# Kernel tuning notes

Measured on AMD Instinct MI355X. Metric: run time of the kernel, lower is better.

The kernel has to match this reference:

```python
import jax, jax.numpy as jnp
import numpy as np

N, E, D, H, G, C = 50000, 800000, 128, 128, 256, 10
BN_EPS = 1e-5

def _lin_init(key, fan_in, fan_out):
    k1, k2 = jax.random.split(key)
    bound = 1.0 / np.sqrt(fan_in)
    w = jax.random.uniform(k1, (fan_in, fan_out), jnp.float32, -bound, bound)
    b = jax.random.uniform(k2, (fan_out,), jnp.float32, -bound, bound)
    return w, b

def setup_inputs() -> dict:
    key = jax.random.key(0)
    ks = jax.random.split(key, 16)
    x = jax.random.normal(ks[0], (N, D), jnp.float32)
    edge_index = jax.random.randint(ks[1], (2, E), 0, N, jnp.int64)
    batch = jnp.sort(jax.random.randint(ks[2], (N,), 0, G, jnp.int64))
    inp = {"x": x, "edge_index": edge_index, "batch": batch}
    # per-layer GIN MLP params: Linear-ReLU-Linear-ReLU-BN
    dims = [(D, H), (H, H), (H, H)]
    for i, (din, dh) in enumerate(dims, start=1):
        wa, ba = _lin_init(ks[2 + 2 * i], din, dh)
        wb, bb = _lin_init(ks[3 + 2 * i], dh, dh)
        inp[f"w{i}a"], inp[f"b{i}a"] = wa, ba
        inp[f"w{i}b"], inp[f"b{i}b"] = wb, bb
        inp[f"g{i}"] = jnp.ones((dh,), jnp.float32)
        inp[f"bt{i}"] = jnp.zeros((dh,), jnp.float32)
    inp["eps"] = jnp.zeros((3,), jnp.float32)  # train_eps=True, init 0
    inp["lw1"], inp["lb1"] = _lin_init(ks[10], H, H)
    inp["lw2"], inp["lb2"] = _lin_init(ks[11], H, C)
    return inp

def _gin_layer(x, src, dst, eps_i, wa, ba, wb, bb, g, bt):
    # scatter-add neighbor aggregation: out[i] = sum_{j->i} x[j]
    agg = jax.ops.segment_sum(x[src], dst, num_segments=N)
    h = (1.0 + eps_i) * x + agg
    h = jax.nn.relu(h @ wa + ba)
    h = jax.nn.relu(h @ wb + bb)
    mu = h.mean(axis=0)
    var = ((h - mu) ** 2).mean(axis=0)  # biased var (torch BN normalization)
    return g * (h - mu) * jax.lax.rsqrt(var + BN_EPS) + bt

def reference(x, edge_index, batch, w1a, b1a, w1b, b1b, g1, bt1,
              w2a, b2a, w2b, b2b, g2, bt2, w3a, b3a, w3b, b3b, g3, bt3,
              eps, lw1, lb1, lw2, lb2):
    src, dst = edge_index[0], edge_index[1]
    h = _gin_layer(x, src, dst, eps[0], w1a, b1a, w1b, b1b, g1, bt1)
    h = _gin_layer(h, src, dst, eps[1], w2a, b2a, w2b, b2b, g2, bt2)
    h = _gin_layer(h, src, dst, eps[2], w3a, b3a, w3b, b3b, g3, bt3)
    # global mean pool over batch ids
    sums = jax.ops.segment_sum(h, batch, num_segments=G)
    cnt = jax.ops.segment_sum(jnp.ones((N,), h.dtype), batch, num_segments=G)
    pooled = sums / jnp.maximum(cnt, 1.0)[:, None]
    z = jax.nn.relu(pooled @ lw1 + lb1)
    # dropout omitted (eval / deterministic reference)
    z = z @ lw2 + lb2
    return jax.nn.log_softmax(z, axis=-1)
```

## Files before the change

### kernel.cpp

```cpp
#include <hip/hip_runtime.h>

#define N_NODES 50000
#define N_EDGES 800000
#define DIM 128
#define N_GRAPHS 256
#define N_CLS 10
#define BN_EPSV 1e-5f
#define CAP 64
#define RSIZE 6250
#define NBLK ((N_NODES + 63) / 64)
#define ZROW N_NODES

typedef __attribute__((ext_vector_type(8))) short short8;
typedef __attribute__((ext_vector_type(4))) float f32x4;

__device__ __forceinline__ float bf2f(short u) {
  return __uint_as_float(((unsigned)(unsigned short)u) << 16);
}
__device__ __forceinline__ unsigned short f2bf(float f) {
  unsigned u = __float_as_uint(f);
  unsigned r = (u + 0x7FFFu + ((u >> 16) & 1u)) >> 16;
  return (unsigned short)r;
}
__device__ __forceinline__ int swz(int row, int bytecol) {
  return row * 256 + (bytecol ^ ((row & 7) << 4));
}


__global__ __launch_bounds__(256) void prep_kernel(
    const float* __restrict__ x, ushort* __restrict__ xb,
    const float* __restrict__ w0, const float* __restrict__ w1,
    const float* __restrict__ w2, const float* __restrict__ w3,
    const float* __restrict__ w4, const float* __restrict__ w5,
    ushort* __restrict__ wt, const int* __restrict__ batch,
    int* __restrict__ gstart, int* __restrict__ cnt,
    ushort* __restrict__ z0, ushort* __restrict__ z1) {
  int bid = blockIdx.x, tid = threadIdx.x;
  if (bid < 384) {
    int m = bid >> 6;
    const float* w = m == 0 ? w0 : m == 1 ? w1 : m == 2 ? w2 : m == 3 ? w3
                                                         : m == 4 ? w4 : w5;
    int idx = (bid & 63) * 256 + tid;
    int k = idx >> 7, n = idx & 127;
    wt[m * 16384 + n * 128 + k] = f2bf(w[idx]);
  } else if (bid < 384 + 2048) {
    const int tot = N_NODES * DIM / 4;
    int i = (bid - 384) * 256 + tid;
    for (; i < tot; i += 2048 * 256) {
      float4 v = ((const float4*)x)[i];
      ushort4 o;
      o.x = f2bf(v.x); o.y = f2bf(v.y); o.z = f2bf(v.z); o.w = f2bf(v.w);
      ((ushort4*)xb)[i] = o;
    }
  } else if (bid < 384 + 2048 + 196) {
    int i = (bid - (384 + 2048)) * 256 + tid;
    if (i < N_NODES) {
      cnt[i] = 0;
      int b = batch[i];
      int prev = (i == 0) ? -1 : batch[i - 1];
      for (int g = prev + 1; g <= b; g++) gstart[g] = i;
      if (i == N_NODES - 1)
        for (int g = b + 1; g <= N_GRAPHS; g++) gstart[g] = N_NODES;
    }
  } else {
    if (tid < DIM) {
      z0[(size_t)ZROW * DIM + tid] = 0;
      z1[(size_t)ZROW * DIM + tid] = 0;
    }
  }
}


__global__ __launch_bounds__(256) void fill_kernel(
    const int* __restrict__ src, const int* __restrict__ dst,
    int* __restrict__ cnt, ushort* __restrict__ csr) {
  int cls = blockIdx.x & 7;
  int lo = cls * RSIZE;
  int hi = lo + RSIZE;
  int i = (blockIdx.x >> 3) * blockDim.x + threadIdx.x;
  int stride = (gridDim.x >> 3) * blockDim.x;
  for (; i < N_EDGES; i += stride) {
    int d = dst[i];
    if (d >= lo && d < hi) {
      int p = atomicAdd(&cnt[d], 1);
      if (p < CAP) csr[(size_t)d * CAP + p] = (ushort)src[i];
    }
  }
}


template <bool FIRST>
__global__ __launch_bounds__(512, 8) void layer_kernel(
    const ushort* __restrict__ xin, const int* __restrict__ cnt,
    const ushort* __restrict__ csr, const float* __restrict__ pstats,
    const float* __restrict__ pgamma, const float* __restrict__ pbeta,
    const float* __restrict__ epsp, int layer,
    const ushort* __restrict__ W1T, const float* __restrict__ b1,
    const ushort* __restrict__ W2T, const float* __restrict__ b2,
    ushort* __restrict__ out, float* __restrict__ bstat) {
  __shared__ __align__(16) ushort As[64 * DIM];
  __shared__ __align__(16) ushort H1[64 * DIM];
  __shared__ float sums[8 * DIM];
  __shared__ float sqs[8 * DIM];
  int tid = threadIdx.x;
  int w8 = tid >> 6;
  int l = tid & 63, li = l & 15, lg = l >> 4;
  int row0 = blockIdx.x * 64;
  float epv = 1.0f + epsp[layer];
  if (!FIRST) {
    if (tid < DIM) {
      const float invN = 1.0f / N_NODES;
      float mu = pstats[tid] * invN;
      float var = fmaxf(pstats[DIM + tid] * invN - mu * mu, 0.f);
      float sc = pgamma[tid] * rsqrtf(var + BN_EPSV);
      sums[tid] = sc;
      sqs[tid] = pbeta[tid] - mu * sc;
    }
    __syncthreads();
  }
  for (int n = 0; n < 8; n++) {
    int nl = w8 * 8 + n;
    int node = row0 + nl;
    float av[8];
#pragma unroll
    for (int j = 0; j < 8; j++) av[j] = 0.f;
    if (node < N_NODES) {
      int deg = cnt[node];
      deg = deg < CAP ? deg : CAP;
      const ushort* nb = csr + (size_t)node * CAP;
      if (lg == 0) {
        short8 sv = *(const short8*)(xin + (size_t)node * DIM + li * 8);
#pragma unroll
        for (int j = 0; j < 8; j++) av[j] = epv * bf2f(sv[j]);
      }
      int nbat = (deg + 15) >> 4;
      for (int b = 0; b < nbat; b++) {
        int i0 = b * 16 + lg, i1 = i0 + 4, i2 = i0 + 8, i3 = i0 + 12;
        int r0 = nb[i0 < deg ? i0 : 0];
        int r1 = nb[i1 < deg ? i1 : 0];
        int r2 = nb[i2 < deg ? i2 : 0];
        int r3 = nb[i3 < deg ? i3 : 0];
        int j0 = i0 < deg ? r0 : ZROW;
        int j1 = i1 < deg ? r1 : ZROW;
        int j2 = i2 < deg ? r2 : ZROW;
        int j3 = i3 < deg ? r3 : ZROW;
        short8 v0 = *(const short8*)(xin + (size_t)j0 * DIM + li * 8);
        short8 v1 = *(const short8*)(xin + (size_t)j1 * DIM + li * 8);
        short8 v2 = *(const short8*)(xin + (size_t)j2 * DIM + li * 8);
        short8 v3 = *(const short8*)(xin + (size_t)j3 * DIM + li * 8);
#pragma unroll
        for (int j = 0; j < 8; j++)
          av[j] += (bf2f(v0[j]) + bf2f(v1[j])) + (bf2f(v2[j]) + bf2f(v3[j]));
      }
#pragma unroll
      for (int j = 0; j < 8; j++) {
        av[j] += __shfl_xor(av[j], 16, 64);
        av[j] += __shfl_xor(av[j], 32, 64);
      }
      if (!FIRST && lg == 0) {
        float co = epv + (float)deg;
#pragma unroll
        for (int j = 0; j < 8; j++)
          av[j] = sums[li * 8 + j] * av[j] + co * sqs[li * 8 + j];
      }
    }
    if (lg == 0) {
      short8 uv;
#pragma unroll
      for (int j = 0; j < 8; j++) uv[j] = (short)f2bf(av[j]);
      *(short8*)((char*)As + swz(nl, li * 16)) = uv;
    }
  }
  __syncthreads();
  int wg = w8 >> 1;
  int ch = w8 & 1;
  {
    f32x4 acc[4] = {};
    short8 af[4];
#pragma unroll
    for (int ks = 0; ks < 4; ks++)
      af[ks] = *(const short8*)((char*)As + swz(16 * wg + li, ks * 64 + lg * 16));
#pragma unroll
    for (int ct4 = 0; ct4 < 4; ct4++) {
      int ct = ch * 4 + ct4;
      const char* wp = (const char*)W1T + (ct * 16 + li) * 256 + lg * 16;
#pragma unroll
      for (int ks = 0; ks < 4; ks++) {
        short8 bf = *(const short8*)(wp + ks * 64);
        acc[ct4] = __builtin_amdgcn_mfma_f32_16x16x32_bf16(af[ks], bf, acc[ct4], 0, 0, 0);
      }
    }
#pragma unroll
    for (int ct4 = 0; ct4 < 4; ct4++) {
      int ct = ch * 4 + ct4;
      float bv = b1[ct * 16 + li];
#pragma unroll
      for (int r = 0; r < 4; r++) {
        int row = 16 * wg + lg * 4 + r;
        *(ushort*)((char*)H1 + swz(row, (ct * 16 + li) * 2)) =
            f2bf(fmaxf(acc[ct4][r] + bv, 0.f));
      }
    }
  }
  __syncthreads();
  float ss[4] = {0, 0, 0, 0}, sq[4] = {0, 0, 0, 0};
  {
    f32x4 acc[4] = {};
    short8 af[4];
#pragma unroll
    for (int ks = 0; ks < 4; ks++)
      af[ks] = *(const short8*)((char*)H1 + swz(16 * wg + li, ks * 64 + lg * 16));
#pragma unroll
    for (int ct4 = 0; ct4 < 4; ct4++) {
      int ct = ch * 4 + ct4;
      const char* wp = (const char*)W2T + (ct * 16 + li) * 256 + lg * 16;
#pragma unroll
      for (int ks = 0; ks < 4; ks++) {
        short8 bf = *(const short8*)(wp + ks * 64);
        acc[ct4] = __builtin_amdgcn_mfma_f32_16x16x32_bf16(af[ks], bf, acc[ct4], 0, 0, 0);
      }
    }
#pragma unroll
    for (int ct4 = 0; ct4 < 4; ct4++) {
      int ct = ch * 4 + ct4;
      float bv = b2[ct * 16 + li];
#pragma unroll
      for (int r = 0; r < 4; r++) {
        int row = 16 * wg + lg * 4 + r;
        float v = fmaxf(acc[ct4][r] + bv, 0.f);
        *(ushort*)((char*)As + swz(row, (ct * 16 + li) * 2)) = f2bf(v);
        float vm = (row0 + row < N_NODES) ? v : 0.f;
        ss[ct4] += vm;
        sq[ct4] += vm * vm;
      }
    }
  }
#pragma unroll
  for (int ct4 = 0; ct4 < 4; ct4++) {
    ss[ct4] += __shfl_xor(ss[ct4], 16, 64);
    ss[ct4] += __shfl_xor(ss[ct4], 32, 64);
    sq[ct4] += __shfl_xor(sq[ct4], 16, 64);
    sq[ct4] += __shfl_xor(sq[ct4], 32, 64);
  }
  if (l < 16) {
#pragma unroll
    for (int ct4 = 0; ct4 < 4; ct4++) {
      sums[w8 * DIM + (ch * 4 + ct4) * 16 + l] = ss[ct4];
      sqs[w8 * DIM + (ch * 4 + ct4) * 16 + l] = sq[ct4];
      sums[w8 * DIM + ((1 - ch) * 4 + ct4) * 16 + l] = 0.f;
      sqs[w8 * DIM + ((1 - ch) * 4 + ct4) * 16 + l] = 0.f;
    }
  }
  __syncthreads();
  for (int t = tid; t < 1024; t += 512) {
    int row = t >> 4, chunk = t & 15;
    int grow = row0 + row;
    if (grow < N_NODES) {
      short8 v = *(const short8*)((char*)As + swz(row, chunk * 16));
      *(short8*)(out + (size_t)grow * DIM + chunk * 8) = v;
    }
  }
  if (tid < DIM) {
    float t1 = 0.f, t2 = 0.f;
#pragma unroll
    for (int g = 0; g < 8; g++) {
      t1 += sums[g * DIM + tid];
      t2 += sqs[g * DIM + tid];
    }
    bstat[(size_t)blockIdx.x * DIM + tid] = t1;
    bstat[((size_t)NBLK + blockIdx.x) * DIM + tid] = t2;
  }
}


__global__ __launch_bounds__(64) void stats_reduce_kernel(
    const float* __restrict__ bstat, float* __restrict__ stats) {
  int c = blockIdx.x;
  int t = threadIdx.x;
  const float* src = bstat + (c < DIM ? 0 : (size_t)NBLK * DIM) + (c & (DIM - 1));
  float a = 0.f;
  for (int b = t; b < NBLK; b += 64) a += src[(size_t)b * DIM];
#pragma unroll
  for (int m = 32; m >= 1; m >>= 1) a += __shfl_xor(a, m, 64);
  if (t == 0) stats[c] = a;
}


__global__ __launch_bounds__(128) void pool2_kernel(const ushort* __restrict__ h,
    const int* __restrict__ gstart, float* __restrict__ pool) {
  int g = blockIdx.x, t = threadIdx.x;
  int s = gstart[g], e = gstart[g + 1];
  float a0 = 0.f, a1 = 0.f, a2 = 0.f, a3 = 0.f;
  int i = s;
  for (; i + 3 < e; i += 4) {
    a0 += bf2f((short)h[(size_t)(i + 0) * DIM + t]);
    a1 += bf2f((short)h[(size_t)(i + 1) * DIM + t]);
    a2 += bf2f((short)h[(size_t)(i + 2) * DIM + t]);
    a3 += bf2f((short)h[(size_t)(i + 3) * DIM + t]);
  }
  for (; i < e; i++) a0 += bf2f((short)h[(size_t)i * DIM + t]);
  float cn = (float)(e - s);
  if (cn < 1.f) cn = 1.f;
  pool[g * DIM + t] = ((a0 + a1) + (a2 + a3)) / cn;
}


__global__ __launch_bounds__(128) void final_kernel(const float* __restrict__ pool,
    const float* __restrict__ stats3,
    const float* __restrict__ gamma3, const float* __restrict__ beta3,
    const float* __restrict__ lw1, const float* __restrict__ lb1,
    const float* __restrict__ lw2, const float* __restrict__ lb2,
    float* __restrict__ out) {
  int g = blockIdx.x, t = threadIdx.x;
  __shared__ float p[DIM];
  __shared__ float part[2];
  __shared__ float z2[N_CLS];
  const float invN = 1.0f / N_NODES;
  float mu = stats3[t] * invN;
  float var = fmaxf(stats3[DIM + t] * invN - mu * mu, 0.f);
  float sc = gamma3[t] * rsqrtf(var + BN_EPSV);
  float sh = beta3[t] - mu * sc;
  p[t] = sc * pool[g * DIM + t] + sh;
  __syncthreads();
  float acc = lb1[t];
  for (int k = 0; k < DIM; k++) acc += p[k] * lw1[k * DIM + t];
  acc = fmaxf(acc, 0.f);
  for (int c = 0; c < N_CLS; c++) {
    float v = acc * lw2[t * N_CLS + c];
#pragma unroll
    for (int m = 32; m >= 1; m >>= 1) v += __shfl_xor(v, m, 64);
    if ((t & 63) == 0) part[t >> 6] = v;
    __syncthreads();
    if (t == 0) z2[c] = part[0] + part[1] + lb2[c];
    __syncthreads();
  }
  if (t == 0) {
    float mx = -1e30f;
    for (int c = 0; c < N_CLS; c++) mx = fmaxf(mx, z2[c]);
    float sum = 0.f;
    for (int c = 0; c < N_CLS; c++) sum += expf(z2[c] - mx);
    float lse = mx + logf(sum);
    for (int c = 0; c < N_CLS; c++) out[g * N_CLS + c] = z2[c] - lse;
  }
}


extern "C" void kernel_launch(void* const* d_in, const int* in_sizes, int n_in,
                              void* d_out, int out_size, void* d_ws, size_t ws_size,
                              hipStream_t stream) {
  const float* x = (const float*)d_in[0];
  const int* edge = (const int*)d_in[1];
  const int* batch = (const int*)d_in[2];
  const float *w[3][2], *bv[3][2], *gam[3], *bet[3];
  int idx = 3;
  for (int l = 0; l < 3; l++) {
    w[l][0] = (const float*)d_in[idx++]; bv[l][0] = (const float*)d_in[idx++];
    w[l][1] = (const float*)d_in[idx++]; bv[l][1] = (const float*)d_in[idx++];
    gam[l] = (const float*)d_in[idx++];  bet[l] = (const float*)d_in[idx++];
  }
  const float* eps = (const float*)d_in[idx++];
  const float* lw1 = (const float*)d_in[idx++];
  const float* lb1 = (const float*)d_in[idx++];
  const float* lw2 = (const float*)d_in[idx++];
  const float* lb2 = (const float*)d_in[idx++];

  char* ws = (char*)d_ws;
  size_t off_b = 0;
  auto alloc = [&](size_t b) -> char* {
    char* p = ws + off_b;
    off_b += (b + 255) & ~(size_t)255;
    return p;
  };
  int* cnt = (int*)alloc((size_t)N_NODES * 4);
  ushort* csr = (ushort*)alloc((size_t)N_NODES * CAP * 2);
  ushort* P0 = (ushort*)alloc((size_t)(N_NODES + 1) * DIM * 2);
  ushort* P1 = (ushort*)alloc((size_t)(N_NODES + 1) * DIM * 2);
  ushort* wt = (ushort*)alloc((size_t)6 * 16384 * 2);
  float* stats = (float*)alloc(3 * 2 * DIM * 4);
  float* pool = (float*)alloc((size_t)N_GRAPHS * DIM * 4);
  int* gstart = (int*)alloc((size_t)(N_GRAPHS + 1) * 4);
  float* bstat = (float*)alloc((size_t)2 * NBLK * DIM * 4);

  const int* srcp = edge;
  const int* dstp = edge + N_EDGES;
  prep_kernel<<<384 + 2048 + 196 + 1, 256, 0, stream>>>(
      x, P0, w[0][0], w[0][1], w[1][0], w[1][1], w[2][0], w[2][1], wt,
      batch, gstart, cnt, P0, P1);
  fill_kernel<<<2048, 256, 0, stream>>>(srcp, dstp, cnt, csr);

  layer_kernel<true><<<NBLK, 512, 0, stream>>>(
      P0, cnt, csr, nullptr, nullptr, nullptr, eps, 0,
      wt + 0 * 16384, bv[0][0], wt + 1 * 16384, bv[0][1], P1, bstat);
  stats_reduce_kernel<<<256, 64, 0, stream>>>(bstat, stats);
  layer_kernel<false><<<NBLK, 512, 0, stream>>>(
      P1, cnt, csr, stats, gam[0], bet[0], eps, 1,
      wt + 2 * 16384, bv[1][0], wt + 3 * 16384, bv[1][1], P0, bstat);
  stats_reduce_kernel<<<256, 64, 0, stream>>>(bstat, stats + 2 * DIM);
  layer_kernel<false><<<NBLK, 512, 0, stream>>>(
      P0, cnt, csr, stats + 2 * DIM, gam[1], bet[1], eps, 2,
      wt + 4 * 16384, bv[2][0], wt + 5 * 16384, bv[2][1], P1, bstat);
  stats_reduce_kernel<<<256, 64, 0, stream>>>(bstat, stats + 4 * DIM);

  pool2_kernel<<<N_GRAPHS, 128, 0, stream>>>(P1, gstart, pool);
  final_kernel<<<N_GRAPHS, 128, 0, stream>>>(pool, stats + 4 * DIM,
                                             gam[2], bet[2], lw1, lb1, lw2, lb2,
                                             (float*)d_out);
}
```

Measured before the change: 278.0 us.

## Split aggregation from MLP and store features in column-sliced layout

Node features are stored as eight 16-column slices (32 bytes per node per slice), and the fused layer kernel is split into a separate aggregation kernel and an MFMA MLP kernel. Each aggregation block works on one slice, chosen by blockIdx & 7, so each slice's working set is small enough to stay cache-resident during the random neighbor gathers. The cost is an extra round trip of the aggregated features through global memory, one more launch per layer, and smaller 8-byte gathers per lane.

```diff
diff --git a/kernel.cpp b/kernel.cpp
--- a/kernel.cpp
+++ b/kernel.cpp
@@ -10,6 +10,8 @@
 #define RSIZE 6250
 #define NBLK ((N_NODES + 63) / 64)
 #define ZROW N_NODES
+#define SLICE ((N_NODES + 1) * 16)
+#define AGG_WPC 768
 
 typedef __attribute__((ext_vector_type(8))) short short8;
 typedef __attribute__((ext_vector_type(4))) float f32x4;
@@ -43,17 +45,24 @@
     int idx = (bid & 63) * 256 + tid;
     int k = idx >> 7, n = idx & 127;
     wt[m * 16384 + n * 128 + k] = f2bf(w[idx]);
-  } else if (bid < 384 + 2048) {
-    const int tot = N_NODES * DIM / 4;
-    int i = (bid - 384) * 256 + tid;
-    for (; i < tot; i += 2048 * 256) {
-      float4 v = ((const float4*)x)[i];
-      ushort4 o;
-      o.x = f2bf(v.x); o.y = f2bf(v.y); o.z = f2bf(v.z); o.w = f2bf(v.w);
-      ((ushort4*)xb)[i] = o;
-    }
-  } else if (bid < 384 + 2048 + 196) {
-    int i = (bid - (384 + 2048)) * 256 + tid;
+  } else if (bid < 384 + 3125) {
+    int id = (bid - 384) * 256 + tid;
+    if (id < 8 * N_NODES * 2) {
+      int s = id / (N_NODES * 2);
+      int r = id - s * (N_NODES * 2);
+      int node = r >> 1, h = r & 1;
+      const float* src = x + (size_t)node * DIM + s * 16 + h * 8;
+      float4 a = *(const float4*)src;
+      float4 b = *(const float4*)(src + 4);
+      short8 o;
+      o[0] = (short)f2bf(a.x); o[1] = (short)f2bf(a.y);
+      o[2] = (short)f2bf(a.z); o[3] = (short)f2bf(a.w);
+      o[4] = (short)f2bf(b.x); o[5] = (short)f2bf(b.y);
+      o[6] = (short)f2bf(b.z); o[7] = (short)f2bf(b.w);
+      *(short8*)(xb + (size_t)s * SLICE + node * 16 + h * 8) = o;
+    }
+  } else if (bid < 384 + 3125 + 196) {
+    int i = (bid - (384 + 3125)) * 256 + tid;
     if (i < N_NODES) {
       cnt[i] = 0;
       int b = batch[i];
@@ -63,9 +72,10 @@
         for (int g = b + 1; g <= N_GRAPHS; g++) gstart[g] = N_NODES;
     }
   } else {
-    if (tid < DIM) {
-      z0[(size_t)ZROW * DIM + tid] = 0;
-      z1[(size_t)ZROW * DIM + tid] = 0;
+    if (tid < 128) {
+      int s = tid >> 4, cc = tid & 15;
+      z0[(size_t)s * SLICE + (size_t)ZROW * 16 + cc] = 0;
+      z1[(size_t)s * SLICE + (size_t)ZROW * 16 + cc] = 0;
     }
   }
 }
@@ -90,14 +100,102 @@
 
 
 template <bool FIRST>
-__global__ __launch_bounds__(512, 8) void layer_kernel(
+__global__ __launch_bounds__(256, 6) void agg_kernel(
     const ushort* __restrict__ xin, const int* __restrict__ cnt,
     const ushort* __restrict__ csr, const float* __restrict__ pstats,
     const float* __restrict__ pgamma, const float* __restrict__ pbeta,
-    const float* __restrict__ epsp, int layer,
-    const ushort* __restrict__ W1T, const float* __restrict__ b1,
-    const ushort* __restrict__ W2T, const float* __restrict__ b2,
-    ushort* __restrict__ out, float* __restrict__ bstat) {
+    const float* __restrict__ epsp, int layer, ushort* __restrict__ agg) {
+  int c = blockIdx.x & 7;
+  int wv = (blockIdx.x >> 3) * 4 + (threadIdx.x >> 6);
+  int l = threadIdx.x & 63;
+  int slot = l >> 2, colq = l & 3;
+  const ushort* F = xin + (size_t)c * SLICE;
+  ushort* A = agg + (size_t)c * SLICE;
+  float epv = 1.0f + epsp[layer];
+  float sc4[4], sh4[4];
+  if (!FIRST) {
+    const float invN = 1.0f / N_NODES;
+#pragma unroll
+    for (int j = 0; j < 4; j++) {
+      int col = c * 16 + colq * 4 + j;
+      float mu = pstats[col] * invN;
+      float var = fmaxf(pstats[DIM + col] * invN - mu * mu, 0.f);
+      float s = pgamma[col] * rsqrtf(var + BN_EPSV);
+      sc4[j] = s;
+      sh4[j] = pbeta[col] - mu * s;
+    }
+  }
+  for (int nb0 = wv; nb0 < N_NODES; nb0 += AGG_WPC * 4) {
+    int n_[4], d_[4];
+#pragma unroll
+    for (int q = 0; q < 4; q++) {
+      n_[q] = nb0 + AGG_WPC * q;
+      int valid = n_[q] < N_NODES;
+      int ndc = valid ? n_[q] : 0;
+      int dd = cnt[ndc];
+      dd = dd < CAP ? dd : CAP;
+      d_[q] = valid ? dd : 0;
+    }
+    int dmax = max(max(d_[0], d_[1]), max(d_[2], d_[3]));
+    int nbat = (dmax + 15) >> 4;
+    float av[4][4];
+#pragma unroll
+    for (int q = 0; q < 4; q++)
+#pragma unroll
+      for (int j = 0; j < 4; j++) av[q][j] = 0.f;
+    for (int b = 0; b < nbat; b++) {
+      int si = b * 16 + slot;
+#pragma unroll
+      for (int q = 0; q < 4; q++) {
+        int ndc = n_[q] < N_NODES ? n_[q] : 0;
+        int e = csr[(size_t)ndc * CAP + (si < d_[q] ? si : 0)];
+        int j = si < d_[q] ? e : ZROW;
+        ushort4 p = *(const ushort4*)(F + j * 16 + colq * 4);
+        av[q][0] += bf2f((short)p.x);
+        av[q][1] += bf2f((short)p.y);
+        av[q][2] += bf2f((short)p.z);
+        av[q][3] += bf2f((short)p.w);
+      }
+    }
+#pragma unroll
+    for (int q = 0; q < 4; q++)
+#pragma unroll
+      for (int j = 0; j < 4; j++) {
+        av[q][j] += __shfl_xor(av[q][j], 4, 64);
+        av[q][j] += __shfl_xor(av[q][j], 8, 64);
+        av[q][j] += __shfl_xor(av[q][j], 16, 64);
+        av[q][j] += __shfl_xor(av[q][j], 32, 64);
+      }
+    if (slot == 0) {
+#pragma unroll
+      for (int q = 0; q < 4; q++) {
+        if (n_[q] >= N_NODES) continue;
+        ushort4 sv = *(const ushort4*)(F + n_[q] * 16 + colq * 4);
+        float o0 = epv * bf2f((short)sv.x) + av[q][0];
+        float o1 = epv * bf2f((short)sv.y) + av[q][1];
+        float o2 = epv * bf2f((short)sv.z) + av[q][2];
+        float o3 = epv * bf2f((short)sv.w) + av[q][3];
+        if (!FIRST) {
+          float co = epv + (float)d_[q];
+          o0 = sc4[0] * o0 + co * sh4[0];
+          o1 = sc4[1] * o1 + co * sh4[1];
+          o2 = sc4[2] * o2 + co * sh4[2];
+          o3 = sc4[3] * o3 + co * sh4[3];
+        }
+        ushort4 ov;
+        ov.x = f2bf(o0); ov.y = f2bf(o1); ov.z = f2bf(o2); ov.w = f2bf(o3);
+        *(ushort4*)(A + n_[q] * 16 + colq * 4) = ov;
+      }
+    }
+  }
+}
+
+
+__global__ __launch_bounds__(512, 8) void mlp_kernel(
+    const ushort* __restrict__ agg, const ushort* __restrict__ W1T,
+    const float* __restrict__ b1, const ushort* __restrict__ W2T,
+    const float* __restrict__ b2, ushort* __restrict__ out,
+    float* __restrict__ bstat) {
   __shared__ __align__(16) ushort As[64 * DIM];
   __shared__ __align__(16) ushort H1[64 * DIM];
   __shared__ float sums[8 * DIM];
@@ -106,70 +204,14 @@
   int w8 = tid >> 6;
   int l = tid & 63, li = l & 15, lg = l >> 4;
   int row0 = blockIdx.x * 64;
-  float epv = 1.0f + epsp[layer];
-  if (!FIRST) {
-    if (tid < DIM) {
-      const float invN = 1.0f / N_NODES;
-      float mu = pstats[tid] * invN;
-      float var = fmaxf(pstats[DIM + tid] * invN - mu * mu, 0.f);
-      float sc = pgamma[tid] * rsqrtf(var + BN_EPSV);
-      sums[tid] = sc;
-      sqs[tid] = pbeta[tid] - mu * sc;
-    }
-    __syncthreads();
-  }
-  for (int n = 0; n < 8; n++) {
-    int nl = w8 * 8 + n;
-    int node = row0 + nl;
-    float av[8];
-#pragma unroll
-    for (int j = 0; j < 8; j++) av[j] = 0.f;
-    if (node < N_NODES) {
-      int deg = cnt[node];
-      deg = deg < CAP ? deg : CAP;
-      const ushort* nb = csr + (size_t)node * CAP;
-      if (lg == 0) {
-        short8 sv = *(const short8*)(xin + (size_t)node * DIM + li * 8);
-#pragma unroll
-        for (int j = 0; j < 8; j++) av[j] = epv * bf2f(sv[j]);
-      }
-      int nbat = (deg + 15) >> 4;
-      for (int b = 0; b < nbat; b++) {
-        int i0 = b * 16 + lg, i1 = i0 + 4, i2 = i0 + 8, i3 = i0 + 12;
-        int r0 = nb[i0 < deg ? i0 : 0];
-        int r1 = nb[i1 < deg ? i1 : 0];
-        int r2 = nb[i2 < deg ? i2 : 0];
-        int r3 = nb[i3 < deg ? i3 : 0];
-        int j0 = i0 < deg ? r0 : ZROW;
-        int j1 = i1 < deg ? r1 : ZROW;
-        int j2 = i2 < deg ? r2 : ZROW;
-        int j3 = i3 < deg ? r3 : ZROW;
-        short8 v0 = *(const short8*)(xin + (size_t)j0 * DIM + li * 8);
-        short8 v1 = *(const short8*)(xin + (size_t)j1 * DIM + li * 8);
-        short8 v2 = *(const short8*)(xin + (size_t)j2 * DIM + li * 8);
-        short8 v3 = *(const short8*)(xin + (size_t)j3 * DIM + li * 8);
-#pragma unroll
-        for (int j = 0; j < 8; j++)
-          av[j] += (bf2f(v0[j]) + bf2f(v1[j])) + (bf2f(v2[j]) + bf2f(v3[j]));
-      }
-#pragma unroll
-      for (int j = 0; j < 8; j++) {
-        av[j] += __shfl_xor(av[j], 16, 64);
-        av[j] += __shfl_xor(av[j], 32, 64);
-      }
-      if (!FIRST && lg == 0) {
-        float co = epv + (float)deg;
-#pragma unroll
-        for (int j = 0; j < 8; j++)
-          av[j] = sums[li * 8 + j] * av[j] + co * sqs[li * 8 + j];
-      }
-    }
-    if (lg == 0) {
-      short8 uv;
-#pragma unroll
-      for (int j = 0; j < 8; j++) uv[j] = (short)f2bf(av[j]);
-      *(short8*)((char*)As + swz(nl, li * 16)) = uv;
-    }
+  for (int t = tid; t < 1024; t += 512) {
+    int s = t >> 7, idx = t & 127;
+    int nl = idx >> 1, h = idx & 1;
+    int grow = row0 + nl;
+    short8 v = {};
+    if (grow < N_NODES)
+      v = *(const short8*)(agg + (size_t)s * SLICE + grow * 16 + h * 8);
+    *(short8*)((char*)As + swz(nl, s * 32 + h * 16)) = v;
   }
   __syncthreads();
   int wg = w8 >> 1;
@@ -253,11 +295,12 @@
   }
   __syncthreads();
   for (int t = tid; t < 1024; t += 512) {
-    int row = t >> 4, chunk = t & 15;
-    int grow = row0 + row;
+    int s = t >> 7, idx = t & 127;
+    int nl = idx >> 1, h = idx & 1;
+    int grow = row0 + nl;
     if (grow < N_NODES) {
-      short8 v = *(const short8*)((char*)As + swz(row, chunk * 16));
-      *(short8*)(out + (size_t)grow * DIM + chunk * 8) = v;
+      short8 v = *(const short8*)((char*)As + swz(nl, s * 32 + h * 16));
+      *(short8*)(out + (size_t)s * SLICE + grow * 16 + h * 8) = v;
     }
   }
   if (tid < DIM) {
@@ -289,17 +332,19 @@
 __global__ __launch_bounds__(128) void pool2_kernel(const ushort* __restrict__ h,
     const int* __restrict__ gstart, float* __restrict__ pool) {
   int g = blockIdx.x, t = threadIdx.x;
-  int s = gstart[g], e = gstart[g + 1];
+  int s = t >> 4, cc = t & 15;
+  const ushort* H = h + (size_t)s * SLICE + cc;
+  int st = gstart[g], e = gstart[g + 1];
   float a0 = 0.f, a1 = 0.f, a2 = 0.f, a3 = 0.f;
-  int i = s;
+  int i = st;
   for (; i + 3 < e; i += 4) {
-    a0 += bf2f((short)h[(size_t)(i + 0) * DIM + t]);
-    a1 += bf2f((short)h[(size_t)(i + 1) * DIM + t]);
-    a2 += bf2f((short)h[(size_t)(i + 2) * DIM + t]);
-    a3 += bf2f((short)h[(size_t)(i + 3) * DIM + t]);
-  }
-  for (; i < e; i++) a0 += bf2f((short)h[(size_t)i * DIM + t]);
-  float cn = (float)(e - s);
+    a0 += bf2f((short)H[(i + 0) * 16]);
+    a1 += bf2f((short)H[(i + 1) * 16]);
+    a2 += bf2f((short)H[(i + 2) * 16]);
+    a3 += bf2f((short)H[(i + 3) * 16]);
+  }
+  for (; i < e; i++) a0 += bf2f((short)H[i * 16]);
+  float cn = (float)(e - st);
   if (cn < 1.f) cn = 1.f;
   pool[g * DIM + t] = ((a0 + a1) + (a2 + a3)) / cn;
 }
@@ -373,8 +418,9 @@
   };
   int* cnt = (int*)alloc((size_t)N_NODES * 4);
   ushort* csr = (ushort*)alloc((size_t)N_NODES * CAP * 2);
-  ushort* P0 = (ushort*)alloc((size_t)(N_NODES + 1) * DIM * 2);
-  ushort* P1 = (ushort*)alloc((size_t)(N_NODES + 1) * DIM * 2);
+  ushort* P0 = (ushort*)alloc((size_t)8 * SLICE * 2);
+  ushort* P1 = (ushort*)alloc((size_t)8 * SLICE * 2);
+  ushort* aggb = (ushort*)alloc((size_t)8 * SLICE * 2);
   ushort* wt = (ushort*)alloc((size_t)6 * 16384 * 2);
   float* stats = (float*)alloc(3 * 2 * DIM * 4);
   float* pool = (float*)alloc((size_t)N_GRAPHS * DIM * 4);
@@ -383,22 +429,25 @@
 
   const int* srcp = edge;
   const int* dstp = edge + N_EDGES;
-  prep_kernel<<<384 + 2048 + 196 + 1, 256, 0, stream>>>(
+  prep_kernel<<<384 + 3125 + 196 + 1, 256, 0, stream>>>(
       x, P0, w[0][0], w[0][1], w[1][0], w[1][1], w[2][0], w[2][1], wt,
       batch, gstart, cnt, P0, P1);
   fill_kernel<<<2048, 256, 0, stream>>>(srcp, dstp, cnt, csr);
 
-  layer_kernel<true><<<NBLK, 512, 0, stream>>>(
-      P0, cnt, csr, nullptr, nullptr, nullptr, eps, 0,
-      wt + 0 * 16384, bv[0][0], wt + 1 * 16384, bv[0][1], P1, bstat);
+  agg_kernel<true><<<1536, 256, 0, stream>>>(
+      P0, cnt, csr, nullptr, nullptr, nullptr, eps, 0, aggb);
+  mlp_kernel<<<NBLK, 512, 0, stream>>>(aggb, wt + 0 * 16384, bv[0][0],
+                                       wt + 1 * 16384, bv[0][1], P1, bstat);
   stats_reduce_kernel<<<256, 64, 0, stream>>>(bstat, stats);
-  layer_kernel<false><<<NBLK, 512, 0, stream>>>(
-      P1, cnt, csr, stats, gam[0], bet[0], eps, 1,
-      wt + 2 * 16384, bv[1][0], wt + 3 * 16384, bv[1][1], P0, bstat);
+  agg_kernel<false><<<1536, 256, 0, stream>>>(
+      P1, cnt, csr, stats, gam[0], bet[0], eps, 1, aggb);
+  mlp_kernel<<<NBLK, 512, 0, stream>>>(aggb, wt + 2 * 16384, bv[1][0],
+                                       wt + 3 * 16384, bv[1][1], P0, bstat);
   stats_reduce_kernel<<<256, 64, 0, stream>>>(bstat, stats + 2 * DIM);
-  layer_kernel<false><<<NBLK, 512, 0, stream>>>(
-      P0, cnt, csr, stats + 2 * DIM, gam[1], bet[1], eps, 2,
-      wt + 4 * 16384, bv[2][0], wt + 5 * 16384, bv[2][1], P1, bstat);
+  agg_kernel<false><<<1536, 256, 0, stream>>>(
+      P0, cnt, csr, stats + 2 * DIM, gam[1], bet[1], eps, 2, aggb);
+  mlp_kernel<<<NBLK, 512, 0, stream>>>(aggb, wt + 4 * 16384, bv[2][0],
+                                       wt + 5 * 16384, bv[2][1], P1, bstat);
   stats_reduce_kernel<<<256, 64, 0, stream>>>(bstat, stats + 4 * DIM);
 
   pool2_kernel<<<N_GRAPHS, 128, 0, stream>>>(P1, gstart, pool);
```

New measurement: 517.9 us. +86.3%, slower.
